# Kernel tuning notes

Measured on AMD Instinct MI355X. Metric: run time of the kernel, lower is better.

## Reference

```python
import jax, jax.numpy as jnp
import numpy as np

B, L, H, S, D = 2, 4096, 16, 64, 128  # batch, seq, num_heads, num_states, head_dim


def setup_inputs() -> dict:
    key = jax.random.key(0)
    k1, k2, k3 = jax.random.split(key, 3)
    return {
        "x": jax.random.normal(k1, (B, L, H, D), dtype=jnp.float32),
        "weight": jax.random.normal(k2, (H, S, D), dtype=jnp.float32),   # nn.Parameter torch.randn
        "bias": jax.random.normal(k3, (H, S), dtype=jnp.float32),
    }


def reference(x, weight, bias):
    b, l, h, d = x.shape
    s = weight.shape[1]
    T = b * l
    # per-head linear router in fp32 (matches x.float()/weight.float() in torch)
    logits = jnp.einsum('blhd,hsd->blhs', x.astype(jnp.float32), weight.astype(jnp.float32)) \
             + bias.astype(jnp.float32)
    score = jax.nn.softmax(logits, axis=-1)                # [B,L,H,S]
    indices = jnp.argmax(score, axis=-1).astype(jnp.int32)  # [B,L,H]
    # GradTop1 forward: all-ones; straight-through backward scatters grad at argmax.
    top = jnp.take_along_axis(score, indices[..., None], axis=-1)[..., 0]
    sg_indices = top - jax.lax.stop_gradient(top) + 1.0      # forward == 1, grad -> one-hot scatter
    # histogram per head over num_states (Triton bincount equivalent)
    flat = indices.reshape(T, h)                             # [T,H]
    counts = jax.vmap(lambda v: jnp.bincount(v, length=s))(flat.T)  # [H,S]
    mean_indices = counts.astype(jnp.float32) / T
    balance_loss = s * jnp.sum(jnp.mean(mean_indices[None, None] * score, axis=(0, 1)))
    return sg_indices.astype(x.dtype), indices, balance_loss.astype(x.dtype)
```

## Files before the change

### kernel.cpp

```cpp
#include <hip/hip_runtime.h>


#define TOKENS  8192
#define NHEAD   16
#define NSTATE  64
#define DDIM    128
#define TH      (TOKENS * NHEAD)
#define WFRAG_BYTES (1u << 19)

typedef _Float16 half8 __attribute__((ext_vector_type(8)));
typedef float    f32x4 __attribute__((ext_vector_type(4)));

constexpr int TPW   = 16;
constexpr int WAVES = 4;
constexpr int TPB   = TPW * WAVES;
constexpr int BPH   = TOKENS / TPB;
constexpr int NBLK  = NHEAD * BPH;

#define GLOAD_LDS16(gsrc, ldst)                                           \
    __builtin_amdgcn_global_load_lds(                                     \
        (const __attribute__((address_space(1))) void*)(gsrc),            \
        (__attribute__((address_space(3))) void*)(ldst), 16, 0, 0)

__device__ __forceinline__ unsigned int ordf(float f) {
    unsigned int u = __float_as_uint(f);
    return (u & 0x80000000u) ? ~u : (u | 0x80000000u);
}

__device__ __forceinline__ void split8(const f32x4 v0, const f32x4 v1,
                                       half8& hh, half8& ll) {
    #pragma unroll
    for (int j = 0; j < 4; ++j) {
        _Float16 h0 = (_Float16)v0[j];
        hh[j]     = h0;  ll[j]     = (_Float16)(v0[j] - (float)h0);
        _Float16 h1 = (_Float16)v1[j];
        hh[4 + j] = h1;  ll[4 + j] = (_Float16)(v1[j] - (float)h1);
    }
}

__global__ __launch_bounds__(256)
void prep_w(const float* __restrict__ w, half8* __restrict__ wfrag)
{
    const int t    = blockIdx.x * 256 + threadIdx.x;
    const int lane = t & 63;
    const int n    = (t >> 6) & 3;
    const int ks   = (t >> 8) & 3;
    const int h    = t >> 10;
    const int s    = n * 16 + (lane & 15);
    const int k0   = ks * 32 + (lane >> 4) * 8;
    const float* src = w + (size_t)(h * NSTATE + s) * DDIM + k0;
    f32x4 v0 = *reinterpret_cast<const f32x4*>(src);
    f32x4 v1 = *reinterpret_cast<const f32x4*>(src + 4);
    half8 hv, lv;
    split8(v0, v1, hv, lv);
    const size_t hb = (size_t)h * 2048;
    const int fb = (ks * 4 + n) * 2;
    wfrag[hb + (size_t)fb * 64 + lane]       = hv;
    wfrag[hb + (size_t)(fb + 1) * 64 + lane] = lv;
}

__global__ __launch_bounds__(256)
void router_mfma(const float* __restrict__ x,
                 const half8* __restrict__ wfrag,
                 const float* __restrict__ bias,
                 float* __restrict__ out,
                 float* __restrict__ ws_sums,
                 int*   __restrict__ ws_cnts)
{
    __shared__ __align__(16) unsigned char smem[32768];

    const int blk  = blockIdx.x;
    const int h    = blk & 15;
    const int bi   = blk >> 4;
    const int tid  = threadIdx.x;
    const int wave = __builtin_amdgcn_readfirstlane(tid >> 6);
    const int lane = tid & 63;
    const int col  = lane & 15;
    const int kg   = lane >> 4;
    const int tokb = bi * TPB + wave * TPW;

    const size_t srow = (size_t)(NHEAD * DDIM);
    const float* arow = x + (size_t)(tokb + col) * srow + h * DDIM + kg * 8;

    f32x4 g[4][2];
    #pragma unroll
    for (int ks = 0; ks < 4; ++ks) {
        g[ks][0] = *reinterpret_cast<const f32x4*>(arow + ks * 32);
        g[ks][1] = *reinterpret_cast<const f32x4*>(arow + ks * 32 + 4);
    }

    {
        const char* wsrc = (const char*)wfrag + (size_t)h * 32768;
        #pragma unroll
        for (int i = 0; i < 8; ++i) {
            const int off = (wave * 8 + i) * 1024;
            GLOAD_LDS16(wsrc + off + lane * 16, smem + off);
        }
    }

    __syncthreads();

    f32x4 acc[4];
    #pragma unroll
    for (int n = 0; n < 4; ++n) {
        f32x4 z = {0.f, 0.f, 0.f, 0.f};
        acc[n] = z;
    }

    #pragma unroll
    for (int ks = 0; ks < 4; ++ks) {
        half8 ah, al;
        split8(g[ks][0], g[ks][1], ah, al);
        #pragma unroll
        for (int n = 0; n < 4; ++n) {
            const int fo = (ks * 4 + n) * 2048 + lane * 16;
            half8 bh = *reinterpret_cast<const half8*>(smem + fo);
            half8 bl = *reinterpret_cast<const half8*>(smem + fo + 1024);
            acc[n] = __builtin_amdgcn_mfma_f32_16x16x32_f16(ah, bh, acc[n], 0, 0, 0);
            acc[n] = __builtin_amdgcn_mfma_f32_16x16x32_f16(ah, bl, acc[n], 0, 0, 0);
            acc[n] = __builtin_amdgcn_mfma_f32_16x16x32_f16(al, bh, acc[n], 0, 0, 0);
        }
    }

    const float b0 = bias[h * NSTATE +  0 + col];
    const float b1 = bias[h * NSTATE + 16 + col];
    const float b2 = bias[h * NSTATE + 32 + col];
    const float b3 = bias[h * NSTATE + 48 + col];

    float sc[4] = {0.f, 0.f, 0.f, 0.f};
    int   cn[4] = {0, 0, 0, 0};

    #pragma unroll
    for (int rg = 0; rg < 4; ++rg) {
        float L0 = acc[0][rg] + b0;
        float L1 = acc[1][rg] + b1;
        float L2 = acc[2][rg] + b2;
        float L3 = acc[3][rg] + b3;

        unsigned long long k0 = ((unsigned long long)ordf(L0) << 6) | (unsigned)(63 - ( 0 + col));
        unsigned long long k1 = ((unsigned long long)ordf(L1) << 6) | (unsigned)(63 - (16 + col));
        unsigned long long k2 = ((unsigned long long)ordf(L2) << 6) | (unsigned)(63 - (32 + col));
        unsigned long long k3 = ((unsigned long long)ordf(L3) << 6) | (unsigned)(63 - (48 + col));
        unsigned long long ka = k0 > k1 ? k0 : k1;
        unsigned long long kb = k2 > k3 ? k2 : k3;
        unsigned long long kk = ka > kb ? ka : kb;
        #pragma unroll
        for (int d = 1; d <= 8; d <<= 1) {
            unsigned long long o = __shfl_xor(kk, d);
            kk = kk > o ? kk : o;
        }
        const int idx = 63 - (int)(kk & 63ull);

        float e0 = __expf(L0), e1 = __expf(L1), e2 = __expf(L2), e3 = __expf(L3);
        float sm = (e0 + e1) + (e2 + e3);
        #pragma unroll
        for (int d = 1; d <= 8; d <<= 1) sm += __shfl_xor(sm, d);
        const float rinv = __builtin_amdgcn_rcpf(sm);
        sc[0] += e0 * rinv; sc[1] += e1 * rinv;
        sc[2] += e2 * rinv; sc[3] += e3 * rinv;

        cn[0] += (idx ==  0 + col);
        cn[1] += (idx == 16 + col);
        cn[2] += (idx == 32 + col);
        cn[3] += (idx == 48 + col);

        if (col == 0) {
            const int t = tokb + (kg << 2) + rg;
            out[(size_t)t * NHEAD + h] = 1.0f;
            out[(size_t)TH + (size_t)t * NHEAD + h] = (float)idx;
        }
    }

    #pragma unroll
    for (int n = 0; n < 4; ++n) {
        sc[n] += __shfl_xor(sc[n], 16);
        sc[n] += __shfl_xor(sc[n], 32);
        cn[n] += __shfl_xor(cn[n], 16);
        cn[n] += __shfl_xor(cn[n], 32);
    }

    __syncthreads();
    float* redf = (float*)smem;
    int*   redi = (int*)(smem + 1024);
    if (kg == 0) {
        #pragma unroll
        for (int n = 0; n < 4; ++n) {
            redf[wave * 64 + n * 16 + col] = sc[n];
            redi[wave * 64 + n * 16 + col] = cn[n];
        }
    }
    __syncthreads();
    if (wave == 0) {
        const float s = redf[lane] + redf[64 + lane] + redf[128 + lane] + redf[192 + lane];
        const int   c = redi[lane] + redi[64 + lane] + redi[128 + lane] + redi[192 + lane];
        atomicAdd(ws_sums + h * NSTATE + lane, s);
        atomicAdd(ws_cnts + h * NSTATE + lane, c);
    }
}

__global__ void router_loss(const float* __restrict__ ws_sums,
                            const int*   __restrict__ ws_cnts,
                            float* __restrict__ out)
{
    const int tid = threadIdx.x;
    float part = 0.0f;
    for (int j = tid; j < NHEAD * NSTATE; j += 256)
        part += (float)ws_cnts[j] * ws_sums[j];

    #pragma unroll
    for (int k = 32; k >= 1; k >>= 1)
        part += __shfl_xor(part, k);

    __shared__ float red[4];
    const int wv = tid >> 6, lane = tid & 63;
    if (lane == 0) red[wv] = part;
    __syncthreads();
    if (tid == 0) {
        const float tot = red[0] + red[1] + red[2] + red[3];
        const float T = (float)TOKENS;
        out[2 * (size_t)TH] = tot * ((float)NSTATE / (T * T));
    }
}

extern "C" void kernel_launch(void* const* d_in, const int* in_sizes, int n_in,
                              void* d_out, int out_size, void* d_ws, size_t ws_size,
                              hipStream_t stream)
{
    const float* x    = (const float*)d_in[0];
    const float* w    = (const float*)d_in[1];
    const float* bias = (const float*)d_in[2];
    float* out = (float*)d_out;

    half8* wfrag   = (half8*)d_ws;
    float* ws_sums = (float*)((char*)d_ws + WFRAG_BYTES);
    int*   ws_cnts = (int*)((char*)d_ws + WFRAG_BYTES + 4096);

    hipMemsetAsync((char*)d_ws + WFRAG_BYTES, 0, 8192, stream);

    prep_w<<<dim3(64), dim3(256), 0, stream>>>(w, wfrag);
    router_mfma<<<dim3(NBLK), dim3(256), 0, stream>>>(x, wfrag, bias, out,
                                                      ws_sums, ws_cnts);
    router_loss<<<dim3(1), dim3(256), 0, stream>>>(ws_sums, ws_cnts, out);
}
```

Before: 34.94 us.

## Loop over four token tiles per block with register double-buffered x loads

Each block now handles 256 tokens per head in four iterations instead of 64, cutting the grid from 2048 to 512 blocks. The weight fragments staged in LDS are reused across the four tiles. The next tile's x values are loaded into a second register buffer while the current tile runs MFMA and softmax, so global load latency overlaps compute. This also means fewer atomics per head-state. In exchange, register pressure rises and there is less block-level parallelism. The LDS array grew to 48KB although only 32KB is used, which may reduce occupancy.

Measured after the change: 35.17 us. No clear change (+0.7%).

```diff
diff --git a/kernel.cpp b/kernel.cpp
--- a/kernel.cpp
+++ b/kernel.cpp
@@ -13,9 +13,8 @@
 
 constexpr int TPW   = 16;
 constexpr int WAVES = 4;
-constexpr int TPB   = TPW * WAVES;
-constexpr int BPH   = TOKENS / TPB;
-constexpr int NBLK  = NHEAD * BPH;
+constexpr int ITERS = 4;
+constexpr int NBLK  = 512;
 
 #define GLOAD_LDS16(gsrc, ldst)                                           \
     __builtin_amdgcn_global_load_lds(                                     \
@@ -67,26 +66,26 @@
                  float* __restrict__ ws_sums,
                  int*   __restrict__ ws_cnts)
 {
-    __shared__ __align__(16) unsigned char smem[32768];
+    __shared__ __align__(16) unsigned char smem[49152];
 
     const int blk  = blockIdx.x;
     const int h    = blk & 15;
-    const int bi   = blk >> 4;
+    const int w0   = blk >> 4;
     const int tid  = threadIdx.x;
     const int wave = __builtin_amdgcn_readfirstlane(tid >> 6);
     const int lane = tid & 63;
     const int col  = lane & 15;
     const int kg   = lane >> 4;
-    const int tokb = bi * TPB + wave * TPW;
+    const int base = w0 * 256 + wave * TPW;
 
     const size_t srow = (size_t)(NHEAD * DDIM);
-    const float* arow = x + (size_t)(tokb + col) * srow + h * DDIM + kg * 8;
-
-    f32x4 g[4][2];
+    const float* arow0 = x + (size_t)(base + col) * srow + h * DDIM + kg * 8;
+
+    f32x4 gA[4][2], gB[4][2];
     #pragma unroll
     for (int ks = 0; ks < 4; ++ks) {
-        g[ks][0] = *reinterpret_cast<const f32x4*>(arow + ks * 32);
-        g[ks][1] = *reinterpret_cast<const f32x4*>(arow + ks * 32 + 4);
+        gA[ks][0] = *reinterpret_cast<const f32x4*>(arow0 + ks * 32);
+        gA[ks][1] = *reinterpret_cast<const f32x4*>(arow0 + ks * 32 + 4);
     }
 
     {
@@ -95,30 +94,6 @@
         for (int i = 0; i < 8; ++i) {
             const int off = (wave * 8 + i) * 1024;
             GLOAD_LDS16(wsrc + off + lane * 16, smem + off);
-        }
-    }
-
-    __syncthreads();
-
-    f32x4 acc[4];
-    #pragma unroll
-    for (int n = 0; n < 4; ++n) {
-        f32x4 z = {0.f, 0.f, 0.f, 0.f};
-        acc[n] = z;
-    }
-
-    #pragma unroll
-    for (int ks = 0; ks < 4; ++ks) {
-        half8 ah, al;
-        split8(g[ks][0], g[ks][1], ah, al);
-        #pragma unroll
-        for (int n = 0; n < 4; ++n) {
-            const int fo = (ks * 4 + n) * 2048 + lane * 16;
-            half8 bh = *reinterpret_cast<const half8*>(smem + fo);
-            half8 bl = *reinterpret_cast<const half8*>(smem + fo + 1024);
-            acc[n] = __builtin_amdgcn_mfma_f32_16x16x32_f16(ah, bh, acc[n], 0, 0, 0);
-            acc[n] = __builtin_amdgcn_mfma_f32_16x16x32_f16(ah, bl, acc[n], 0, 0, 0);
-            acc[n] = __builtin_amdgcn_mfma_f32_16x16x32_f16(al, bh, acc[n], 0, 0, 0);
         }
     }
 
@@ -127,47 +102,86 @@
     const float b2 = bias[h * NSTATE + 32 + col];
     const float b3 = bias[h * NSTATE + 48 + col];
 
+    __syncthreads();
+
     float sc[4] = {0.f, 0.f, 0.f, 0.f};
     int   cn[4] = {0, 0, 0, 0};
 
     #pragma unroll
-    for (int rg = 0; rg < 4; ++rg) {
-        float L0 = acc[0][rg] + b0;
-        float L1 = acc[1][rg] + b1;
-        float L2 = acc[2][rg] + b2;
-        float L3 = acc[3][rg] + b3;
-
-        unsigned long long k0 = ((unsigned long long)ordf(L0) << 6) | (unsigned)(63 - ( 0 + col));
-        unsigned long long k1 = ((unsigned long long)ordf(L1) << 6) | (unsigned)(63 - (16 + col));
-        unsigned long long k2 = ((unsigned long long)ordf(L2) << 6) | (unsigned)(63 - (32 + col));
-        unsigned long long k3 = ((unsigned long long)ordf(L3) << 6) | (unsigned)(63 - (48 + col));
-        unsigned long long ka = k0 > k1 ? k0 : k1;
-        unsigned long long kb = k2 > k3 ? k2 : k3;
-        unsigned long long kk = ka > kb ? ka : kb;
-        #pragma unroll
-        for (int d = 1; d <= 8; d <<= 1) {
-            unsigned long long o = __shfl_xor(kk, d);
-            kk = kk > o ? kk : o;
-        }
-        const int idx = 63 - (int)(kk & 63ull);
-
-        float e0 = __expf(L0), e1 = __expf(L1), e2 = __expf(L2), e3 = __expf(L3);
-        float sm = (e0 + e1) + (e2 + e3);
-        #pragma unroll
-        for (int d = 1; d <= 8; d <<= 1) sm += __shfl_xor(sm, d);
-        const float rinv = __builtin_amdgcn_rcpf(sm);
-        sc[0] += e0 * rinv; sc[1] += e1 * rinv;
-        sc[2] += e2 * rinv; sc[3] += e3 * rinv;
-
-        cn[0] += (idx ==  0 + col);
-        cn[1] += (idx == 16 + col);
-        cn[2] += (idx == 32 + col);
-        cn[3] += (idx == 48 + col);
-
-        if (col == 0) {
-            const int t = tokb + (kg << 2) + rg;
-            out[(size_t)t * NHEAD + h] = 1.0f;
-            out[(size_t)TH + (size_t)t * NHEAD + h] = (float)idx;
+    for (int it = 0; it < ITERS; ++it) {
+        f32x4 (&gc)[4][2] = (it & 1) ? gB : gA;
+        f32x4 (&gn)[4][2] = (it & 1) ? gA : gB;
+
+        if (it < ITERS - 1) {
+            const float* arow = arow0 + (size_t)(it + 1) * 64 * srow;
+            #pragma unroll
+            for (int ks = 0; ks < 4; ++ks) {
+                gn[ks][0] = *reinterpret_cast<const f32x4*>(arow + ks * 32);
+                gn[ks][1] = *reinterpret_cast<const f32x4*>(arow + ks * 32 + 4);
+            }
+        }
+
+        f32x4 acc[4];
+        #pragma unroll
+        for (int n = 0; n < 4; ++n) {
+            f32x4 z = {0.f, 0.f, 0.f, 0.f};
+            acc[n] = z;
+        }
+        #pragma unroll
+        for (int ks = 0; ks < 4; ++ks) {
+            half8 ah, al;
+            split8(gc[ks][0], gc[ks][1], ah, al);
+            #pragma unroll
+            for (int n = 0; n < 4; ++n) {
+                const int fo = (ks * 4 + n) * 2048 + lane * 16;
+                half8 bh = *reinterpret_cast<const half8*>(smem + fo);
+                half8 bl = *reinterpret_cast<const half8*>(smem + fo + 1024);
+                acc[n] = __builtin_amdgcn_mfma_f32_16x16x32_f16(ah, bh, acc[n], 0, 0, 0);
+                acc[n] = __builtin_amdgcn_mfma_f32_16x16x32_f16(ah, bl, acc[n], 0, 0, 0);
+                acc[n] = __builtin_amdgcn_mfma_f32_16x16x32_f16(al, bh, acc[n], 0, 0, 0);
+            }
+        }
+
+        const int tokb = base + it * 64;
+        #pragma unroll
+        for (int rg = 0; rg < 4; ++rg) {
+            float L0 = acc[0][rg] + b0;
+            float L1 = acc[1][rg] + b1;
+            float L2 = acc[2][rg] + b2;
+            float L3 = acc[3][rg] + b3;
+
+            unsigned long long k0 = ((unsigned long long)ordf(L0) << 6) | (unsigned)(63 - ( 0 + col));
+            unsigned long long k1 = ((unsigned long long)ordf(L1) << 6) | (unsigned)(63 - (16 + col));
+            unsigned long long k2 = ((unsigned long long)ordf(L2) << 6) | (unsigned)(63 - (32 + col));
+            unsigned long long k3 = ((unsigned long long)ordf(L3) << 6) | (unsigned)(63 - (48 + col));
+            unsigned long long ka = k0 > k1 ? k0 : k1;
+            unsigned long long kb = k2 > k3 ? k2 : k3;
+            unsigned long long kk = ka > kb ? ka : kb;
+            #pragma unroll
+            for (int d = 1; d <= 8; d <<= 1) {
+                unsigned long long o = __shfl_xor(kk, d);
+                kk = kk > o ? kk : o;
+            }
+            const int idx = 63 - (int)(kk & 63ull);
+
+            float e0 = __expf(L0), e1 = __expf(L1), e2 = __expf(L2), e3 = __expf(L3);
+            float sm = (e0 + e1) + (e2 + e3);
+            #pragma unroll
+            for (int d = 1; d <= 8; d <<= 1) sm += __shfl_xor(sm, d);
+            const float rinv = __builtin_amdgcn_rcpf(sm);
+            sc[0] += e0 * rinv; sc[1] += e1 * rinv;
+            sc[2] += e2 * rinv; sc[3] += e3 * rinv;
+
+            cn[0] += (idx ==  0 + col);
+            cn[1] += (idx == 16 + col);
+            cn[2] += (idx == 32 + col);
+            cn[3] += (idx == 48 + col);
+
+            if (col == 0) {
+                const int t = tokb + (kg << 2) + rg;
+                out[(size_t)t * NHEAD + h] = 1.0f;
+                out[(size_t)TH + (size_t)t * NHEAD + h] = (float)idx;
+            }
         }
     }
 
```

## Persistent-style router blocks with double-buffered LDS x staging and register-resident weights

Applied to the files above, without the earlier changes.

Each block now handles 256 tokens of one head: every wave loops over four 16-token tiles, staging x into swizzled LDS with async global-to-LDS loads, double-buffered and gated by manual vmcnt waits, while the weight fragments stay in registers. The memset is removed by having prep_w zero the replicated reduction buffers, and atomics are spread over 8 replicas to reduce contention. The scattered per-token index and one writes move into a finale kernel that transposes through LDS so the output stores are coalesced; that kernel also computes the loss. This adds register pressure from 32 half8 weight fragments plus an extra scratch round trip for the indices.

After: 36.85 us. 5.5% more time.

```diff
diff --git a/kernel.cpp b/kernel.cpp
--- a/kernel.cpp
+++ b/kernel.cpp
@@ -6,16 +6,14 @@
 #define NSTATE  64
 #define DDIM    128
 #define TH      (TOKENS * NHEAD)
+
 #define WFRAG_BYTES (1u << 19)
+#define REP_OFF     WFRAG_BYTES
+#define REP_BYTES   65536
+#define IDX_OFF     (WFRAG_BYTES + REP_BYTES)
 
 typedef _Float16 half8 __attribute__((ext_vector_type(8)));
 typedef float    f32x4 __attribute__((ext_vector_type(4)));
-
-constexpr int TPW   = 16;
-constexpr int WAVES = 4;
-constexpr int TPB   = TPW * WAVES;
-constexpr int BPH   = TOKENS / TPB;
-constexpr int NBLK  = NHEAD * BPH;
 
 #define GLOAD_LDS16(gsrc, ldst)                                           \
     __builtin_amdgcn_global_load_lds(                                     \
@@ -39,9 +37,11 @@
 }
 
 __global__ __launch_bounds__(256)
-void prep_w(const float* __restrict__ w, half8* __restrict__ wfrag)
+void prep_w(const float* __restrict__ w, half8* __restrict__ wfrag,
+            float* __restrict__ rep )
 {
     const int t    = blockIdx.x * 256 + threadIdx.x;
+    rep[t] = 0.0f;
     const int lane = t & 63;
     const int n    = (t >> 6) & 3;
     const int ks   = (t >> 8) & 3;
@@ -59,68 +59,47 @@
     wfrag[hb + (size_t)(fb + 1) * 64 + lane] = lv;
 }
 
-__global__ __launch_bounds__(256)
+__global__ __launch_bounds__(256, 2)
 void router_mfma(const float* __restrict__ x,
                  const half8* __restrict__ wfrag,
                  const float* __restrict__ bias,
-                 float* __restrict__ out,
-                 float* __restrict__ ws_sums,
-                 int*   __restrict__ ws_cnts)
-{
-    __shared__ __align__(16) unsigned char smem[32768];
+                 float* __restrict__ idx_scr,
+                 float* __restrict__ repf,
+                 float* __restrict__ repc)
+{
+    __shared__ __align__(16) unsigned char smem[65536];
 
     const int blk  = blockIdx.x;
     const int h    = blk & 15;
-    const int bi   = blk >> 4;
+    const int win  = blk >> 4;
     const int tid  = threadIdx.x;
     const int wave = __builtin_amdgcn_readfirstlane(tid >> 6);
     const int lane = tid & 63;
     const int col  = lane & 15;
     const int kg   = lane >> 4;
-    const int tokb = bi * TPB + wave * TPW;
-
+    const int base = win * 256 + wave * 64;
+
+    unsigned char* const Aw = smem + wave * 16384;
     const size_t srow = (size_t)(NHEAD * DDIM);
-    const float* arow = x + (size_t)(tokb + col) * srow + h * DDIM + kg * 8;
-
-    f32x4 g[4][2];
-    #pragma unroll
-    for (int ks = 0; ks < 4; ++ks) {
-        g[ks][0] = *reinterpret_cast<const f32x4*>(arow + ks * 32);
-        g[ks][1] = *reinterpret_cast<const f32x4*>(arow + ks * 32 + 4);
-    }
-
-    {
-        const char* wsrc = (const char*)wfrag + (size_t)h * 32768;
+
+    auto stageA = [&](int it, int buf) {
+        const int tokb = base + it * 16;
+        unsigned char* dst = Aw + buf * 8192;
         #pragma unroll
         for (int i = 0; i < 8; ++i) {
-            const int off = (wave * 8 + i) * 1024;
-            GLOAD_LDS16(wsrc + off + lane * 16, smem + off);
-        }
-    }
-
-    __syncthreads();
-
-    f32x4 acc[4];
-    #pragma unroll
-    for (int n = 0; n < 4; ++n) {
-        f32x4 z = {0.f, 0.f, 0.f, 0.f};
-        acc[n] = z;
-    }
-
-    #pragma unroll
-    for (int ks = 0; ks < 4; ++ks) {
-        half8 ah, al;
-        split8(g[ks][0], g[ks][1], ah, al);
-        #pragma unroll
-        for (int n = 0; n < 4; ++n) {
-            const int fo = (ks * 4 + n) * 2048 + lane * 16;
-            half8 bh = *reinterpret_cast<const half8*>(smem + fo);
-            half8 bl = *reinterpret_cast<const half8*>(smem + fo + 1024);
-            acc[n] = __builtin_amdgcn_mfma_f32_16x16x32_f16(ah, bh, acc[n], 0, 0, 0);
-            acc[n] = __builtin_amdgcn_mfma_f32_16x16x32_f16(ah, bl, acc[n], 0, 0, 0);
-            acc[n] = __builtin_amdgcn_mfma_f32_16x16x32_f16(al, bh, acc[n], 0, 0, 0);
-        }
-    }
+            const int r = i * 2 + (lane >> 5);
+            const float* src = x + (size_t)(tokb + r) * srow + h * DDIM
+                             + 4 * ((lane & 31) ^ (r & 7));
+            GLOAD_LDS16(src, dst + i * 1024);
+        }
+    };
+
+    stageA(0, 0);
+
+    half8 breg[32];
+    #pragma unroll
+    for (int f = 0; f < 32; ++f)
+        breg[f] = wfrag[(size_t)h * 2048 + (size_t)f * 64 + lane];
 
     const float b0 = bias[h * NSTATE +  0 + col];
     const float b1 = bias[h * NSTATE + 16 + col];
@@ -131,44 +110,76 @@
     int   cn[4] = {0, 0, 0, 0};
 
     #pragma unroll
-    for (int rg = 0; rg < 4; ++rg) {
-        float L0 = acc[0][rg] + b0;
-        float L1 = acc[1][rg] + b1;
-        float L2 = acc[2][rg] + b2;
-        float L3 = acc[3][rg] + b3;
-
-        unsigned long long k0 = ((unsigned long long)ordf(L0) << 6) | (unsigned)(63 - ( 0 + col));
-        unsigned long long k1 = ((unsigned long long)ordf(L1) << 6) | (unsigned)(63 - (16 + col));
-        unsigned long long k2 = ((unsigned long long)ordf(L2) << 6) | (unsigned)(63 - (32 + col));
-        unsigned long long k3 = ((unsigned long long)ordf(L3) << 6) | (unsigned)(63 - (48 + col));
-        unsigned long long ka = k0 > k1 ? k0 : k1;
-        unsigned long long kb = k2 > k3 ? k2 : k3;
-        unsigned long long kk = ka > kb ? ka : kb;
-        #pragma unroll
-        for (int d = 1; d <= 8; d <<= 1) {
-            unsigned long long o = __shfl_xor(kk, d);
-            kk = kk > o ? kk : o;
-        }
-        const int idx = 63 - (int)(kk & 63ull);
-
-        float e0 = __expf(L0), e1 = __expf(L1), e2 = __expf(L2), e3 = __expf(L3);
-        float sm = (e0 + e1) + (e2 + e3);
-        #pragma unroll
-        for (int d = 1; d <= 8; d <<= 1) sm += __shfl_xor(sm, d);
-        const float rinv = __builtin_amdgcn_rcpf(sm);
-        sc[0] += e0 * rinv; sc[1] += e1 * rinv;
-        sc[2] += e2 * rinv; sc[3] += e3 * rinv;
-
-        cn[0] += (idx ==  0 + col);
-        cn[1] += (idx == 16 + col);
-        cn[2] += (idx == 32 + col);
-        cn[3] += (idx == 48 + col);
-
-        if (col == 0) {
-            const int t = tokb + (kg << 2) + rg;
-            out[(size_t)t * NHEAD + h] = 1.0f;
-            out[(size_t)TH + (size_t)t * NHEAD + h] = (float)idx;
-        }
+    for (int it = 0; it < 4; ++it) {
+        const int buf = it & 1;
+        if (it < 3) stageA(it + 1, buf ^ 1);
+        if (it == 0)      asm volatile("s_waitcnt vmcnt(8)" ::: "memory");
+        else if (it < 3)  asm volatile("s_waitcnt vmcnt(9)" ::: "memory");
+        else              asm volatile("s_waitcnt vmcnt(1)" ::: "memory");
+
+        f32x4 acc[4];
+        #pragma unroll
+        for (int n = 0; n < 4; ++n) {
+            f32x4 z = {0.f, 0.f, 0.f, 0.f};
+            acc[n] = z;
+        }
+
+        #pragma unroll
+        for (int ks = 0; ks < 4; ++ks) {
+            const int s0 = ks * 8 + kg * 2;
+            const unsigned char* ab = Aw + buf * 8192 + col * 512;
+            f32x4 a0 = *reinterpret_cast<const f32x4*>(ab + 16 * ( s0      ^ (col & 7)));
+            f32x4 a1 = *reinterpret_cast<const f32x4*>(ab + 16 * ((s0 + 1) ^ (col & 7)));
+            half8 ah, al;
+            split8(a0, a1, ah, al);
+            #pragma unroll
+            for (int n = 0; n < 4; ++n) {
+                acc[n] = __builtin_amdgcn_mfma_f32_16x16x32_f16(ah, breg[(ks*4+n)*2],     acc[n], 0, 0, 0);
+                acc[n] = __builtin_amdgcn_mfma_f32_16x16x32_f16(ah, breg[(ks*4+n)*2 + 1], acc[n], 0, 0, 0);
+                acc[n] = __builtin_amdgcn_mfma_f32_16x16x32_f16(al, breg[(ks*4+n)*2],     acc[n], 0, 0, 0);
+            }
+        }
+
+        const int tokb = base + it * 16;
+        int my_idx = 0;
+        #pragma unroll
+        for (int rg = 0; rg < 4; ++rg) {
+            float L0 = acc[0][rg] + b0;
+            float L1 = acc[1][rg] + b1;
+            float L2 = acc[2][rg] + b2;
+            float L3 = acc[3][rg] + b3;
+
+            unsigned long long k0 = ((unsigned long long)ordf(L0) << 6) | (unsigned)(63 - ( 0 + col));
+            unsigned long long k1 = ((unsigned long long)ordf(L1) << 6) | (unsigned)(63 - (16 + col));
+            unsigned long long k2 = ((unsigned long long)ordf(L2) << 6) | (unsigned)(63 - (32 + col));
+            unsigned long long k3 = ((unsigned long long)ordf(L3) << 6) | (unsigned)(63 - (48 + col));
+            unsigned long long ka = k0 > k1 ? k0 : k1;
+            unsigned long long kb = k2 > k3 ? k2 : k3;
+            unsigned long long kk = ka > kb ? ka : kb;
+            #pragma unroll
+            for (int d = 1; d <= 8; d <<= 1) {
+                unsigned long long o = __shfl_xor(kk, d);
+                kk = kk > o ? kk : o;
+            }
+            const int idx = 63 - (int)(kk & 63ull);
+
+            float e0 = __expf(L0), e1 = __expf(L1), e2 = __expf(L2), e3 = __expf(L3);
+            float sm = (e0 + e1) + (e2 + e3);
+            #pragma unroll
+            for (int d = 1; d <= 8; d <<= 1) sm += __shfl_xor(sm, d);
+            const float rinv = __builtin_amdgcn_rcpf(sm);
+            sc[0] += e0 * rinv; sc[1] += e1 * rinv;
+            sc[2] += e2 * rinv; sc[3] += e3 * rinv;
+
+            cn[0] += (idx ==  0 + col);
+            cn[1] += (idx == 16 + col);
+            cn[2] += (idx == 32 + col);
+            cn[3] += (idx == 48 + col);
+
+            if (col == rg) my_idx = idx;
+        }
+        if (col < 4)
+            idx_scr[(size_t)h * TOKENS + tokb + (kg << 2) + col] = (float)my_idx;
     }
 
     #pragma unroll
@@ -178,47 +189,60 @@
         cn[n] += __shfl_xor(cn[n], 16);
         cn[n] += __shfl_xor(cn[n], 32);
     }
-
-    __syncthreads();
-    float* redf = (float*)smem;
-    int*   redi = (int*)(smem + 1024);
     if (kg == 0) {
+        const int rep = ((blk << 2) | wave) & 7;
         #pragma unroll
         for (int n = 0; n < 4; ++n) {
-            redf[wave * 64 + n * 16 + col] = sc[n];
-            redi[wave * 64 + n * 16 + col] = cn[n];
-        }
-    }
-    __syncthreads();
-    if (wave == 0) {
-        const float s = redf[lane] + redf[64 + lane] + redf[128 + lane] + redf[192 + lane];
-        const int   c = redi[lane] + redi[64 + lane] + redi[128 + lane] + redi[192 + lane];
-        atomicAdd(ws_sums + h * NSTATE + lane, s);
-        atomicAdd(ws_cnts + h * NSTATE + lane, c);
-    }
-}
-
-__global__ void router_loss(const float* __restrict__ ws_sums,
-                            const int*   __restrict__ ws_cnts,
-                            float* __restrict__ out)
-{
+            atomicAdd(repf + rep * 1024 + h * 64 + n * 16 + col, sc[n]);
+            atomicAdd(repc + rep * 1024 + h * 64 + n * 16 + col, (float)cn[n]);
+        }
+    }
+}
+
+__global__ __launch_bounds__(256)
+void finale(const float* __restrict__ idx_scr,
+            const float* __restrict__ repf,
+            const float* __restrict__ repc,
+            float* __restrict__ out)
+{
+    const int b   = blockIdx.x;
     const int tid = threadIdx.x;
-    float part = 0.0f;
-    for (int j = tid; j < NHEAD * NSTATE; j += 256)
-        part += (float)ws_cnts[j] * ws_sums[j];
-
-    #pragma unroll
-    for (int k = 32; k >= 1; k >>= 1)
-        part += __shfl_xor(part, k);
-
-    __shared__ float red[4];
-    const int wv = tid >> 6, lane = tid & 63;
-    if (lane == 0) red[wv] = part;
-    __syncthreads();
-    if (tid == 0) {
-        const float tot = red[0] + red[1] + red[2] + red[3];
-        const float T = (float)TOKENS;
-        out[2 * (size_t)TH] = tot * ((float)NSTATE / (T * T));
+
+    if (b < 32) {
+        __shared__ float tl[256 * 17];
+        #pragma unroll
+        for (int hh = 0; hh < 16; ++hh)
+            tl[tid * 17 + hh] = idx_scr[(size_t)hh * TOKENS + b * 256 + tid];
+        __syncthreads();
+        #pragma unroll
+        for (int k = 0; k < 16; ++k) {
+            const int i = k * 256 + tid;
+            out[(size_t)TH + (size_t)b * 4096 + i] = tl[(i >> 4) * 17 + (i & 15)];
+            out[(size_t)b * 4096 + i] = 1.0f;
+        }
+    } else {
+        float part = 0.0f;
+        for (int j = tid; j < NHEAD * NSTATE; j += 256) {
+            float cf = 0.f, cc = 0.f;
+            #pragma unroll
+            for (int r = 0; r < 8; ++r) {
+                cf += repf[r * 1024 + j];
+                cc += repc[r * 1024 + j];
+            }
+            part += cf * cc;
+        }
+        #pragma unroll
+        for (int d = 1; d <= 32; d <<= 1)
+            part += __shfl_xor(part, d);
+        __shared__ float red[4];
+        const int wv = tid >> 6, lane = tid & 63;
+        if (lane == 0) red[wv] = part;
+        __syncthreads();
+        if (tid == 0) {
+            const float tot = red[0] + red[1] + red[2] + red[3];
+            const float T = (float)TOKENS;
+            out[2 * (size_t)TH] = tot * ((float)NSTATE / (T * T));
+        }
     }
 }
 
@@ -232,13 +256,13 @@
     float* out = (float*)d_out;
 
     half8* wfrag   = (half8*)d_ws;
-    float* ws_sums = (float*)((char*)d_ws + WFRAG_BYTES);
-    int*   ws_cnts = (int*)((char*)d_ws + WFRAG_BYTES + 4096);
-
-    hipMemsetAsync((char*)d_ws + WFRAG_BYTES, 0, 8192, stream);
-
-    prep_w<<<dim3(64), dim3(256), 0, stream>>>(w, wfrag);
-    router_mfma<<<dim3(NBLK), dim3(256), 0, stream>>>(x, wfrag, bias, out,
-                                                      ws_sums, ws_cnts);
-    router_loss<<<dim3(1), dim3(256), 0, stream>>>(ws_sums, ws_cnts, out);
-}
+    float* rep     = (float*)((char*)d_ws + REP_OFF);
+    float* repf    = rep;
+    float* repc    = rep + 8192;
+    float* idx_scr = (float*)((char*)d_ws + IDX_OFF);
+
+    prep_w<<<dim3(64), dim3(256), 0, stream>>>(w, wfrag, rep);
+    router_mfma<<<dim3(512), dim3(256), 0, stream>>>(x, wfrag, bias,
+                                                     idx_scr, repf, repc);
+    finale<<<dim3(33), dim3(256), 0, stream>>>(idx_scr, repf, repc, out);
+}
```
